# Performance work log

Hardware: AMD Instinct MI355X
Metric: run time of the kernel (lower is better)

## Reference

```python
import jax, jax.numpy as jnp
import numpy as np

B, D, K = 65536, 128, 8
BOUND = 3.0
MIN_BIN_W = 1e-3   # min_bin_width
MIN_BIN_H = 1e-3   # min_bin_height
MIN_DERIV = 1e-3   # min_derivative
EPS = 1e-6


def setup_inputs() -> dict:
    key = jax.random.key(0)
    k1, k2, k3, k4 = jax.random.split(key, 4)
    return {
        "x": jax.random.normal(k1, (B, D), jnp.float32) * 1.5,
        "unnormalized_widths": jax.random.normal(k2, (D, K), jnp.float32),
        "unnormalized_heights": jax.random.normal(k3, (D, K), jnp.float32),
        "unnormalized_derivatives": jax.random.normal(k4, (D, K - 1), jnp.float32),
    }


def _calculate_knots(lengths, lower, upper):
    # lengths: [D, K] summing to ~1 -> scaled lengths and knot positions [D, K+1]
    knots = jnp.cumsum(lengths, axis=-1)
    knots = jnp.pad(knots, ((0, 0), (1, 0)))
    knots = (upper - lower) * knots + lower
    knots = knots.at[..., 0].set(lower)
    knots = knots.at[..., -1].set(upper)
    return knots[..., 1:] - knots[..., :-1], knots


def _select_bins(p, idx):
    # p: [D, Kp] per-dim tables, idx: [B, D] bin indices -> [B, D]
    i = jnp.clip(idx, 0, p.shape[-1] - 1)
    return p[jnp.arange(p.shape[0])[None, :], i]


def _spline_forward(x, uw, uh, ud):
    w = jax.nn.softmax(uw, axis=-1)
    h = jax.nn.softmax(uh, axis=-1)
    d = jax.nn.softplus(ud)

    num_bins = w.shape[-1]
    widths = MIN_BIN_W + (1.0 - MIN_BIN_W * num_bins) * w
    heights = MIN_BIN_H + (1.0 - MIN_BIN_H * num_bins) * h
    derivs = jnp.pad(MIN_DERIV + d, ((0, 0), (1, 1)), constant_values=1.0 - MIN_DERIV)  # [D, K+1]

    widths, cumwidths = _calculate_knots(widths, -BOUND, BOUND)
    heights, cumheights = _calculate_knots(heights, -BOUND, BOUND)

    inside = (x >= -BOUND) & (x <= BOUND)
    xc = jnp.clip(x, -BOUND, BOUND)  # keep tail values finite; masked out below

    # searchsorted: which bin each input falls into   [B, D]
    bin_idx = jnp.sum(xc[..., None] >= (cumwidths + EPS)[None, :, :], axis=-1) - 1

    iw = _select_bins(widths, bin_idx)
    icw = _select_bins(cumwidths, bin_idx)
    ich = _select_bins(cumheights, bin_idx)
    idelta = _select_bins(heights / widths, bin_idx)
    id0 = _select_bins(derivs, bin_idx)
    id1 = _select_bins(derivs[..., 1:], bin_idx)
    ih = _select_bins(heights, bin_idx)

    # rational quadratic spline (forward)
    theta = (xc - icw) / iw
    t1m = theta * (1.0 - theta)
    numerator = ih * (idelta * theta ** 2 + id0 * t1m)
    denominator = idelta + (id0 + id1 - 2.0 * idelta) * t1m
    out = ich + numerator / denominator
    dnum = idelta ** 2 * (id1 * theta ** 2 + 2.0 * idelta * t1m + id0 * (1.0 - theta) ** 2)
    lad = jnp.log(dnum) - 2.0 * jnp.log(denominator)

    u = jnp.where(inside, out, x)          # identity outside tail bound
    lad = jnp.where(inside, lad, 0.0)
    return u, lad


def reference(x, unnormalized_widths, unnormalized_heights, unnormalized_derivatives):
    u, lad = _spline_forward(x, unnormalized_widths, unnormalized_heights, unnormalized_derivatives)
    log_detJ = jnp.sum(lad, axis=1)
    return u, log_detJ
```

## Files before the change

### kernel.cpp

```cpp
#include <hip/hip_runtime.h>
#include <math.h>

namespace {
constexpr int D = 128;
constexpr int K = 8;
constexpr float BOUND = 3.0f;
constexpr float EPS = 1e-6f;
constexpr float MIN_BIN_W = 1e-3f;
constexpr float MIN_BIN_H = 1e-3f;
constexpr float MIN_DERIV = 1e-3f;
constexpr float LN2 = 0.6931471805599453f;
constexpr int REC = 8;
constexpr int S = K * REC + 4;
constexpr int WPB = 4;
constexpr int PPW = 4;
}

__device__ __forceinline__ float spline_elem(float xv, const float* __restrict__ row,
                                             const float* kn, float* __restrict__ outp) {
    const bool inside = (xv >= -BOUND) & (xv <= BOUND);
    const float xc = fminf(fmaxf(xv, -BOUND), BOUND);
    int idx = 0;
    #pragma unroll
    for (int j = 0; j < 7; ++j) idx += (xc >= kn[j]) ? 1 : 0;
    const float4 ra = *(const float4*)(row + idx * REC);
    const float4 rb = *(const float4*)(row + idx * REC + 4);
    const float theta = (xc - ra.x) * ra.y;
    const float omt   = 1.f - theta;
    const float t1m   = theta * omt;
    const float th2   = theta * theta;
    const float num   = rb.y * (ra.w * th2 + ra.z * t1m);
    const float den   = ra.w + rb.w * t1m;
    const float rd    = __builtin_amdgcn_rcpf(den);
    const float outv  = fmaf(num, rd, rb.x);
    const float dnum  = ra.w * ra.w * (rb.z * th2 + 2.f * ra.w * t1m + ra.z * omt * omt);
    const float lad   = __log2f(dnum * rd * rd);
    *outp = inside ? outv : xv;
    return inside ? lad : 0.f;
}

__global__ __launch_bounds__(256) void spline_fwd(
    const float* __restrict__ x,
    const float* __restrict__ uw,
    const float* __restrict__ uh,
    const float* __restrict__ ud,
    float* __restrict__ out_u,
    float* __restrict__ out_ld,
    int nrows)
{
    __shared__ __align__(16) float s_tab[D * S];

    const int tid = threadIdx.x;
    if (tid < D) {
        const int d = tid;
        float wv[K], hv[K], cw[K + 1], ch[K + 1], der[K + 1];

        {
            const float* p = uw + d * K;
            float m = p[0];
            #pragma unroll
            for (int j = 1; j < K; ++j) m = fmaxf(m, p[j]);
            float s = 0.f;
            #pragma unroll
            for (int j = 0; j < K; ++j) { wv[j] = __expf(p[j] - m); s += wv[j]; }
            const float inv = 1.f / s;
            #pragma unroll
            for (int j = 0; j < K; ++j)
                wv[j] = MIN_BIN_W + (1.f - MIN_BIN_W * K) * (wv[j] * inv);
        }
        {
            const float* p = uh + d * K;
            float m = p[0];
            #pragma unroll
            for (int j = 1; j < K; ++j) m = fmaxf(m, p[j]);
            float s = 0.f;
            #pragma unroll
            for (int j = 0; j < K; ++j) { hv[j] = __expf(p[j] - m); s += hv[j]; }
            const float inv = 1.f / s;
            #pragma unroll
            for (int j = 0; j < K; ++j)
                hv[j] = MIN_BIN_H + (1.f - MIN_BIN_H * K) * (hv[j] * inv);
        }
        cw[0] = -BOUND; ch[0] = -BOUND;
        float cs_w = 0.f, cs_h = 0.f;
        #pragma unroll
        for (int j = 0; j < K; ++j) {
            cs_w += wv[j]; cw[j + 1] = 2.f * BOUND * cs_w - BOUND;
            cs_h += hv[j]; ch[j + 1] = 2.f * BOUND * cs_h - BOUND;
        }
        cw[K] = BOUND; ch[K] = BOUND;

        der[0] = 1.f - MIN_DERIV;
        der[K] = 1.f - MIN_DERIV;
        {
            const float* p = ud + d * (K - 1);
            #pragma unroll
            for (int j = 1; j < K; ++j) {
                const float v = p[j - 1];
                const float sp = log1pf(__expf(-fabsf(v))) + fmaxf(v, 0.f);
                der[j] = MIN_DERIV + sp;
            }
        }

        float* row = s_tab + ((d & 3) * 32 + (d >> 2)) * S;
        #pragma unroll
        for (int j = 0; j < K; ++j) {
            const float w  = cw[j + 1] - cw[j];
            const float h  = ch[j + 1] - ch[j];
            const float dl = h / w;
            row[j * REC + 0] = cw[j];
            row[j * REC + 1] = 1.f / w;
            row[j * REC + 2] = der[j];
            row[j * REC + 3] = dl;
            row[j * REC + 4] = ch[j];
            row[j * REC + 5] = h;
            row[j * REC + 6] = der[j + 1];
            row[j * REC + 7] = der[j] + der[j + 1] - 2.f * dl;
        }
    }
    __syncthreads();

    const int wave = tid >> 6;
    const int lane = tid & 63;
    const int l32  = lane & 31;
    const int half = lane >> 5;

    const float* rowp0 = s_tab + (0 * 32 + l32) * S;
    const float* rowp1 = s_tab + (1 * 32 + l32) * S;
    const float* rowp2 = s_tab + (2 * 32 + l32) * S;
    const float* rowp3 = s_tab + (3 * 32 + l32) * S;

    float kn[28];
    #pragma unroll
    for (int j = 0; j < 7; ++j) {
        kn[j]      = rowp0[(j + 1) * REC] + EPS;
        kn[7 + j]  = rowp1[(j + 1) * REC] + EPS;
        kn[14 + j] = rowp2[(j + 1) * REC] + EPS;
        kn[21 + j] = rowp3[(j + 1) * REC] + EPS;
    }

    const int npairs = nrows >> 1;
    const int p0 = (blockIdx.x * WPB + wave) * PPW;
    const int lo4 = lane << 2;

    float4 xv[PPW];
    #pragma unroll
    for (int c = 0; c < PPW; ++c) {
        const int p = p0 + c;
        const int pc = (p < npairs) ? p : (npairs - 1);
        xv[c] = *(const float4*)(x + (size_t)(pc * 2) * D + lo4);
    }

    #pragma unroll
    for (int c = 0; c < PPW; ++c) {
        const int p = p0 + c;
        if (p < npairs) {
            float4 u;
            float la;
            la  = spline_elem(xv[c].x, rowp0, kn +  0, &u.x);
            la += spline_elem(xv[c].y, rowp1, kn +  7, &u.y);
            la += spline_elem(xv[c].z, rowp2, kn + 14, &u.z);
            la += spline_elem(xv[c].w, rowp3, kn + 21, &u.w);

            *(float4*)(out_u + (size_t)(p * 2) * D + lo4) = u;

            la += __shfl_xor(la, 1);
            la += __shfl_xor(la, 2);
            la += __shfl_xor(la, 4);
            la += __shfl_xor(la, 8);
            la += __shfl_xor(la, 16);
            if (l32 == 0) out_ld[p * 2 + half] = la * LN2;
        }
    }
}

extern "C" void kernel_launch(void* const* d_in, const int* in_sizes, int n_in,
                              void* d_out, int out_size, void* d_ws, size_t ws_size,
                              hipStream_t stream) {
    const float* x  = (const float*)d_in[0];
    const float* uw = (const float*)d_in[1];
    const float* uh = (const float*)d_in[2];
    const float* ud = (const float*)d_in[3];
    const int nrows = in_sizes[0] / D;
    float* out_u  = (float*)d_out;
    float* out_ld = (float*)d_out + (size_t)nrows * D;
    const int npairs = nrows / 2;
    const int nwaves = (npairs + PPW - 1) / PPW;
    const int nblocks = (nwaves + WPB - 1) / WPB;
    spline_fwd<<<nblocks, 256, 0, stream>>>(x, uw, uh, ud, out_u, out_ld, nrows);
}
```

Before: 102.7 us.

## Double block size, prefetch next row pair, drop bounds checks

Raises the block to 512 threads (8 waves) so each block's per-dimension table setup is amortized over twice as many rows. The up-front load of all four x pairs is replaced by a rolling one-ahead prefetch that lowers register pressure, and the tail bounds checks are removed. A few divisions in the setup become reciprocal multiplies. Dropping the bounds checks assumes the row-pair count divides evenly by 32, and the per-block setup is now done by 128 of 512 threads, which leaves the remaining waves idle during it.

Result: slower. 119.4 us (+16.2%).

```diff
diff --git a/kernel.cpp b/kernel.cpp
--- a/kernel.cpp
+++ b/kernel.cpp
@@ -12,7 +12,7 @@
 constexpr float LN2 = 0.6931471805599453f;
 constexpr int REC = 8;
 constexpr int S = K * REC + 4;
-constexpr int WPB = 4;
+constexpr int WPB = 8;
 constexpr int PPW = 4;
 }
 
@@ -39,7 +39,7 @@
     return inside ? lad : 0.f;
 }
 
-__global__ __launch_bounds__(256) void spline_fwd(
+__global__ __launch_bounds__(512, 8) void spline_fwd(
     const float* __restrict__ x,
     const float* __restrict__ uw,
     const float* __restrict__ uh,
@@ -63,10 +63,9 @@
             float s = 0.f;
             #pragma unroll
             for (int j = 0; j < K; ++j) { wv[j] = __expf(p[j] - m); s += wv[j]; }
-            const float inv = 1.f / s;
+            const float inv = __builtin_amdgcn_rcpf(s) * (1.f - MIN_BIN_W * K);
             #pragma unroll
-            for (int j = 0; j < K; ++j)
-                wv[j] = MIN_BIN_W + (1.f - MIN_BIN_W * K) * (wv[j] * inv);
+            for (int j = 0; j < K; ++j) wv[j] = MIN_BIN_W + wv[j] * inv;
         }
         {
             const float* p = uh + d * K;
@@ -76,10 +75,9 @@
             float s = 0.f;
             #pragma unroll
             for (int j = 0; j < K; ++j) { hv[j] = __expf(p[j] - m); s += hv[j]; }
-            const float inv = 1.f / s;
+            const float inv = __builtin_amdgcn_rcpf(s) * (1.f - MIN_BIN_H * K);
             #pragma unroll
-            for (int j = 0; j < K; ++j)
-                hv[j] = MIN_BIN_H + (1.f - MIN_BIN_H * K) * (hv[j] * inv);
+            for (int j = 0; j < K; ++j) hv[j] = MIN_BIN_H + hv[j] * inv;
         }
         cw[0] = -BOUND; ch[0] = -BOUND;
         float cs_w = 0.f, cs_h = 0.f;
@@ -107,9 +105,10 @@
         for (int j = 0; j < K; ++j) {
             const float w  = cw[j + 1] - cw[j];
             const float h  = ch[j + 1] - ch[j];
-            const float dl = h / w;
+            const float iw = 1.f / w;
+            const float dl = h * iw;
             row[j * REC + 0] = cw[j];
-            row[j * REC + 1] = 1.f / w;
+            row[j * REC + 1] = iw;
             row[j * REC + 2] = der[j];
             row[j * REC + 3] = dl;
             row[j * REC + 4] = ch[j];
@@ -139,38 +138,34 @@
         kn[21 + j] = rowp3[(j + 1) * REC] + EPS;
     }
 
-    const int npairs = nrows >> 1;
     const int p0 = (blockIdx.x * WPB + wave) * PPW;
     const int lo4 = lane << 2;
 
-    float4 xv[PPW];
+    float4 xcur = *(const float4*)(x + (size_t)(p0 * 2) * D + lo4);
     #pragma unroll
     for (int c = 0; c < PPW; ++c) {
         const int p = p0 + c;
-        const int pc = (p < npairs) ? p : (npairs - 1);
-        xv[c] = *(const float4*)(x + (size_t)(pc * 2) * D + lo4);
-    }
+        float4 xnext;
+        if (c + 1 < PPW)
+            xnext = *(const float4*)(x + (size_t)((p + 1) * 2) * D + lo4);
 
-    #pragma unroll
-    for (int c = 0; c < PPW; ++c) {
-        const int p = p0 + c;
-        if (p < npairs) {
-            float4 u;
-            float la;
-            la  = spline_elem(xv[c].x, rowp0, kn +  0, &u.x);
-            la += spline_elem(xv[c].y, rowp1, kn +  7, &u.y);
-            la += spline_elem(xv[c].z, rowp2, kn + 14, &u.z);
-            la += spline_elem(xv[c].w, rowp3, kn + 21, &u.w);
+        float4 u;
+        float la;
+        la  = spline_elem(xcur.x, rowp0, kn +  0, &u.x);
+        la += spline_elem(xcur.y, rowp1, kn +  7, &u.y);
+        la += spline_elem(xcur.z, rowp2, kn + 14, &u.z);
+        la += spline_elem(xcur.w, rowp3, kn + 21, &u.w);
 
-            *(float4*)(out_u + (size_t)(p * 2) * D + lo4) = u;
+        *(float4*)(out_u + (size_t)(p * 2) * D + lo4) = u;
 
-            la += __shfl_xor(la, 1);
-            la += __shfl_xor(la, 2);
-            la += __shfl_xor(la, 4);
-            la += __shfl_xor(la, 8);
-            la += __shfl_xor(la, 16);
-            if (l32 == 0) out_ld[p * 2 + half] = la * LN2;
-        }
+        la += __shfl_xor(la, 1);
+        la += __shfl_xor(la, 2);
+        la += __shfl_xor(la, 4);
+        la += __shfl_xor(la, 8);
+        la += __shfl_xor(la, 16);
+        if (l32 == 0) out_ld[p * 2 + half] = la * LN2;
+
+        xcur = xnext;
     }
 }
 
@@ -185,7 +180,6 @@
     float* out_u  = (float*)d_out;
     float* out_ld = (float*)d_out + (size_t)nrows * D;
     const int npairs = nrows / 2;
-    const int nwaves = (npairs + PPW - 1) / PPW;
-    const int nblocks = (nwaves + WPB - 1) / WPB;
-    spline_fwd<<<nblocks, 256, 0, stream>>>(x, uw, uh, ud, out_u, out_ld, nrows);
+    const int nblocks = (npairs + WPB * PPW - 1) / (WPB * PPW);
+    spline_fwd<<<nblocks, 512, 0, stream>>>(x, uw, uh, ud, out_u, out_ld, nrows);
 }
```
